# Performance work log

Hardware: AMD Instinct MI355X
Metric: run time of the kernel (lower is better)

The kernel has to match this reference:

```python
import jax, jax.numpy as jnp
from jax import lax
import numpy as np

B, T, I, H, O = 256, 1024, 64, 256, 1


def setup_inputs() -> dict:
    key = jax.random.key(0)
    ks = jax.random.split(key, 7)
    s = 0.05
    return {
        "x": jax.random.normal(ks[0], (B, T, I), dtype=jnp.float32),
        "W_ih": jax.random.normal(ks[1], (4 * H, I), dtype=jnp.float32) * s,
        "W_hh": jax.random.normal(ks[2], (4 * H, H), dtype=jnp.float32) * s,
        "b_ih": jax.random.normal(ks[3], (4 * H,), dtype=jnp.float32) * s,
        "b_hh": jax.random.normal(ks[4], (4 * H,), dtype=jnp.float32) * s,
        "fc_w": jax.random.normal(ks[5], (O, H), dtype=jnp.float32) * s,
        "fc_b": jax.random.normal(ks[6], (O,), dtype=jnp.float32) * s,
    }


def _lstm_last_hidden(x, W_ih, W_hh, b_ih, b_hh):
    # x: [B, T, I] -> last hidden state h_T: [B, H]
    h_dim = W_hh.shape[1]
    xT = jnp.swapaxes(x, 0, 1)                      # [T, B, I]
    # Precompute input contribution to gates for all timesteps (one big GEMM)
    x_gates = jnp.einsum("tbi,gi->tbg", xT, W_ih) + b_ih + b_hh  # [T, B, 4H]

    def step(carry, xg):
        h, c = carry
        g = xg + h @ W_hh.T                         # [B, 4H]
        i, f, gg, o = jnp.split(g, 4, axis=-1)       # torch gate order i,f,g,o
        i = jax.nn.sigmoid(i)
        f = jax.nn.sigmoid(f)
        gg = jnp.tanh(gg)
        o = jax.nn.sigmoid(o)
        c = f * c + i * gg
        h = o * jnp.tanh(c)
        return (h, c), None

    b = x.shape[0]
    h0 = jnp.zeros((b, h_dim), dtype=x.dtype)
    c0 = jnp.zeros((b, h_dim), dtype=x.dtype)
    (h_last, _), _ = lax.scan(step, (h0, c0), x_gates)
    return h_last


def reference(x, W_ih, W_hh, b_ih, b_hh, fc_w, fc_b):
    h_last = _lstm_last_hidden(x, W_ih, W_hh, b_ih, b_hh)  # [B, H]
    return h_last @ fc_w.T + fc_b                           # [B, O]
```

## Files before the change

### kernel.cpp

```cpp
#include <hip/hip_runtime.h>
#include <stdint.h>


#define T_ 1024
#define I_ 64
#define H_ 256
#define NSLICE 8
#define NGROUP 32
#define MB 8
#define HB 32
#define HROW 272

#define UNITS_PER_GROUP 1024
#define UNITS_PER_PARITY (NGROUP * UNITS_PER_GROUP)
#define SENT_CAP (1 << 16)

typedef float floatx4 __attribute__((ext_vector_type(4)));
typedef __bf16 bf16x8 __attribute__((ext_vector_type(8)));
typedef unsigned short ushortx8 __attribute__((ext_vector_type(8)));
typedef unsigned int uintx4 __attribute__((ext_vector_type(4)));
typedef unsigned int uint32;
typedef unsigned long long u64;

__device__ __forceinline__ float bf2f(uint32 u16) {
  uint32 u = u16 << 16;
  return __builtin_bit_cast(float, u);
}
__device__ __forceinline__ bf16x8 packbf8(floatx4 a, floatx4 b) {
  bf16x8 r;
  r[0] = (__bf16)a[0]; r[1] = (__bf16)a[1];
  r[2] = (__bf16)a[2]; r[3] = (__bf16)a[3];
  r[4] = (__bf16)b[0]; r[5] = (__bf16)b[1];
  r[6] = (__bf16)b[2]; r[7] = (__bf16)b[3];
  return r;
}
__device__ __forceinline__ float fast_sig(float v) {
  return 1.0f / (1.0f + __expf(-v));
}
__device__ __forceinline__ float fast_tanh(float v) {
  float e = __expf(2.0f * v);
  return 1.0f - 2.0f / (e + 1.0f);
}
__device__ __forceinline__ u64 aload64(const u64* p) {
  return __hip_atomic_load(p, __ATOMIC_RELAXED, __HIP_MEMORY_SCOPE_AGENT);
}
__device__ __forceinline__ void pub64(u64* p, u64 v) {
  asm volatile("global_atomic_swap_x2 %0, %1, off sc1" ::"v"(p), "v"(v)
               : "memory");
}

__global__ __launch_bounds__(256, 1) void lstm_main(
    const float* __restrict__ x, const float* __restrict__ W_ih,
    const float* __restrict__ W_hh, const float* __restrict__ b_ih,
    const float* __restrict__ b_hh, u64* __restrict__ units) {
  const int tid = threadIdx.x;
  const int bid = blockIdx.x;
  const int s = bid >> 5;
  const int g = bid & 31;
  const int w = tid >> 6;
  const int lane = tid & 63;
  const int ln = lane & 15;
  const int lk = lane >> 4;

  __shared__ float xch[4][2][16][8];
  __shared__ __align__(16) unsigned short h_lds[MB][HROW];

  {
    uint32* p = (uint32*)&h_lds[0][0];
    for (int i = tid; i < MB * HROW / 2; i += 256) p[i] = 0u;
  }

  bf16x8 wf[2][10];
  float bias[2];
#pragma unroll
  for (int j = 0; j < 2; ++j) {
    const int row = w * 256 + s * HB + j * 16 + ln;
    bias[j] = b_ih[row] + b_hh[row];
#pragma unroll
    for (int kc = 0; kc < 10; ++kc) {
      const int kk = kc * 32 + lk * 8;
      const float* src = (kk < I_) ? (W_ih + (size_t)row * I_ + kk)
                                   : (W_hh + (size_t)row * H_ + (kk - I_));
      floatx4 f0 = *(const floatx4*)src;
      floatx4 f1 = *(const floatx4*)(src + 4);
      wf[j][kc] = packbf8(f0, f1);
    }
  }

  const int mb = ln & 7;
  const float* xrow = x + ((size_t)(g * MB + mb)) * T_ * I_;
  const int um = tid >> 5;
  const int uh = tid & 31;
  const int uj = uh >> 4, un = uh & 15;
  float c_reg = 0.0f;

  const bool ownthr = (((tid & 31) >> 2) == s);

  const size_t gbase = (size_t)g * UNITS_PER_GROUP;

  __syncthreads();

#pragma unroll 1
  for (int t = 0; t < T_; ++t) {
    floatx4 xf0, xf1, xf2, xf3;
    {
      const float* src = xrow + t * I_ + lk * 8;
      xf0 = *(const floatx4*)(src);
      xf1 = *(const floatx4*)(src + 4);
      xf2 = *(const floatx4*)(src + 32);
      xf3 = *(const floatx4*)(src + 36);
    }

    const u64* up =
        units + (size_t)(t & 1) * UNITS_PER_PARITY + gbase + tid * 4;
    u64 v0 = 0, v1 = 0, v2 = 0, v3 = 0;
    const bool polling = (t > 0) && !ownthr;
    if (polling) {
      v0 = aload64(up + 0);
      v1 = aload64(up + 1);
      v2 = aload64(up + 2);
      v3 = aload64(up + 3);
    }

    bf16x8 a0 = packbf8(xf0, xf1);
    bf16x8 a1 = packbf8(xf2, xf3);
    floatx4 acc[2];
    acc[0] = (floatx4){bias[0], bias[0], bias[0], bias[0]};
    acc[1] = (floatx4){bias[1], bias[1], bias[1], bias[1]};
    acc[0] = __builtin_amdgcn_mfma_f32_16x16x32_bf16(a0, wf[0][0], acc[0],
                                                     0, 0, 0);
    acc[1] = __builtin_amdgcn_mfma_f32_16x16x32_bf16(a0, wf[1][0], acc[1],
                                                     0, 0, 0);
    acc[0] = __builtin_amdgcn_mfma_f32_16x16x32_bf16(a1, wf[0][1], acc[0],
                                                     0, 0, 0);
    acc[1] = __builtin_amdgcn_mfma_f32_16x16x32_bf16(a1, wf[1][1], acc[1],
                                                     0, 0, 0);

    if (t > 0) {
      bool ok = !polling || (((uint32)(v0 >> 32) == (uint32)t) &
                            ((uint32)(v1 >> 32) == (uint32)t) &
                            ((uint32)(v2 >> 32) == (uint32)t) &
                            ((uint32)(v3 >> 32) == (uint32)t));
      int it = 0;
      while (!__all(ok) && ++it < SENT_CAP) {
        if (!ok) {
          v0 = aload64(up + 0);
          v1 = aload64(up + 1);
          v2 = aload64(up + 2);
          v3 = aload64(up + 3);
          ok = ((uint32)(v0 >> 32) == (uint32)t) &
               ((uint32)(v1 >> 32) == (uint32)t) &
               ((uint32)(v2 >> 32) == (uint32)t) &
               ((uint32)(v3 >> 32) == (uint32)t);
        }
      }
      if (polling) {
        uintx4 d;
        d[0] = (uint32)v0; d[1] = (uint32)v1;
        d[2] = (uint32)v2; d[3] = (uint32)v3;
        uint32* dst = (uint32*)&h_lds[tid >> 5][0] + (tid & 31) * 4;
        *(uintx4*)dst = d;
      }
    }
    __syncthreads();

    const unsigned short* hrow = &h_lds[mb][0];
#pragma unroll
    for (int kc = 2; kc < 10; ++kc) {
      bf16x8 a = __builtin_bit_cast(
          bf16x8, *(const ushortx8*)(hrow + (kc - 2) * 32 + lk * 8));
      acc[0] = __builtin_amdgcn_mfma_f32_16x16x32_bf16(a, wf[0][kc], acc[0],
                                                       0, 0, 0);
      acc[1] = __builtin_amdgcn_mfma_f32_16x16x32_bf16(a, wf[1][kc], acc[1],
                                                       0, 0, 0);
    }

#pragma unroll
    for (int j = 0; j < 2; ++j) {
      floatx4 v = acc[j];
      if (w == 2) {
        v[0] = fast_tanh(v[0]); v[1] = fast_tanh(v[1]);
        v[2] = fast_tanh(v[2]); v[3] = fast_tanh(v[3]);
      } else {
        v[0] = fast_sig(v[0]); v[1] = fast_sig(v[1]);
        v[2] = fast_sig(v[2]); v[3] = fast_sig(v[3]);
      }
      if (lk < 2) {
        *(floatx4*)&xch[w][j][ln][lk * 4] = v;
      }
    }
    __syncthreads();

    float ig = xch[0][uj][un][um];
    float fg = xch[1][uj][un][um];
    float gg = xch[2][uj][un][um];
    float og = xch[3][uj][un][um];
    c_reg = fg * c_reg + ig * gg;
    float hv = og * fast_tanh(c_reg);

    unsigned short hb = __builtin_bit_cast(unsigned short, (__bf16)hv);
    int pv = __shfl_xor((int)hb, 1);
    if ((uh & 1) == 0) {
      uint32 dword = (uint32)hb | ((uint32)(unsigned short)pv << 16);
      u64 val = (u64)dword | ((u64)(uint32)(t + 1) << 32);
      u64* dst = units + (size_t)((t + 1) & 1) * UNITS_PER_PARITY + gbase +
                 (um * 128 + s * 16 + (uh >> 1));
      pub64(dst, val);
      *(uint32*)&h_lds[um][2 * (s * 16 + (uh >> 1))] = dword;
    }
  }
}

__global__ void lstm_fc(const u64* __restrict__ units,
                        const float* __restrict__ fc_w,
                        const float* __restrict__ fc_b,
                        float* __restrict__ out) {
  const int b = threadIdx.x;
  const int g = b >> 3, m = b & 7;
  const u64* base = units + (size_t)g * UNITS_PER_GROUP + m * 128;
  float sum = fc_b[0];
#pragma unroll 8
  for (int d = 0; d < 128; ++d) {
    u64 v = aload64(base + d);
    uint32 lo = (uint32)v;
    sum += bf2f(lo & 0xffffu) * fc_w[2 * d] + bf2f(lo >> 16) * fc_w[2 * d + 1];
  }
  out[b] = sum;
}

extern "C" void kernel_launch(void* const* d_in, const int* in_sizes, int n_in,
                              void* d_out, int out_size, void* d_ws,
                              size_t ws_size, hipStream_t stream) {
  const float* x    = (const float*)d_in[0];
  const float* W_ih = (const float*)d_in[1];
  const float* W_hh = (const float*)d_in[2];
  const float* b_ih = (const float*)d_in[3];
  const float* b_hh = (const float*)d_in[4];
  const float* fc_w = (const float*)d_in[5];
  const float* fc_b = (const float*)d_in[6];
  float* out = (float*)d_out;

  u64* units = (u64*)d_ws;

  lstm_main<<<dim3(NGROUP * NSLICE), dim3(256), 0, stream>>>(
      x, W_ih, W_hh, b_ih, b_hh, units);
  lstm_fc<<<dim3(1), dim3(256), 0, stream>>>(units, fc_w, fc_b, out);
}
```

Before: 2.421 ms.

## Add XCC-local fast exchange path with handshake and device-scope fallback

```diff
diff --git a/kernel.cpp b/kernel.cpp
--- a/kernel.cpp
+++ b/kernel.cpp
@@ -12,8 +12,11 @@
 #define HROW 272
 
 #define UNITS_PER_GROUP 1024
-#define UNITS_PER_PARITY (NGROUP * UNITS_PER_GROUP)
+#define UPP (NGROUP * UNITS_PER_GROUP)
 #define SENT_CAP (1 << 16)
+#define FASTCAP 24
+#define HTAG 0x48414E44u
+#define HS_CAP (1 << 20)
 
 typedef float floatx4 __attribute__((ext_vector_type(4)));
 typedef __bf16 bf16x8 __attribute__((ext_vector_type(8)));
@@ -44,9 +47,24 @@
 __device__ __forceinline__ u64 aload64(const u64* p) {
   return __hip_atomic_load(p, __ATOMIC_RELAXED, __HIP_MEMORY_SCOPE_AGENT);
 }
-__device__ __forceinline__ void pub64(u64* p, u64 v) {
-  asm volatile("global_atomic_swap_x2 %0, %1, off sc1" ::"v"(p), "v"(v)
+__device__ __forceinline__ void astore64(u64* p, u64 v) {
+  __hip_atomic_store(p, v, __ATOMIC_RELAXED, __HIP_MEMORY_SCOPE_AGENT);
+}
+__device__ __forceinline__ void pubswap(u64* p, u64 v) {
+  asm volatile("global_atomic_swap_x2 %0, %1, off" ::"v"(p), "v"(v)
                : "memory");
+}
+__device__ __forceinline__ int xcc_id() {
+  int x;
+  asm volatile("s_getreg_b32 %0, hwreg(HW_REG_XCC_ID)" : "=s"(x));
+  return x & 0xf;
+}
+__device__ __forceinline__ bool tags4(u64 v0, u64 v1, u64 v2, u64 v3,
+                                      int t) {
+  return ((uint32)(v0 >> 32) == (uint32)t) &
+         ((uint32)(v1 >> 32) == (uint32)t) &
+         ((uint32)(v2 >> 32) == (uint32)t) &
+         ((uint32)(v3 >> 32) == (uint32)t);
 }
 
 __global__ __launch_bounds__(256, 1) void lstm_main(
@@ -65,6 +83,13 @@
   __shared__ float xch[4][2][16][8];
   __shared__ __align__(16) unsigned short h_lds[MB][HROW];
 
+  const size_t gbase = (size_t)g * UNITS_PER_GROUP;
+
+  if (tid == 0) {
+    u64 hv = (u64)(uint32)xcc_id() | ((u64)HTAG << 32);
+    astore64(units + gbase + s, hv);
+  }
+
   {
     uint32* p = (uint32*)&h_lds[0][0];
     for (int i = tid; i < MB * HROW / 2; i += 256) p[i] = 0u;
@@ -87,6 +112,24 @@
     }
   }
 
+  bool fast;
+  {
+    u64 idv[8] = {0, 0, 0, 0, 0, 0, 0, 0};
+    bool hok = false;
+    for (int it = 0; !hok && it < HS_CAP; ++it) {
+      hok = true;
+#pragma unroll
+      for (int p = 0; p < 8; ++p) {
+        idv[p] = aload64(units + gbase + p);
+        hok &= ((uint32)(idv[p] >> 32) == HTAG);
+      }
+      if (!hok) __builtin_amdgcn_s_sleep(2);
+    }
+    fast = hok;
+#pragma unroll
+    for (int p = 1; p < 8; ++p) fast &= ((uint32)idv[0] == (uint32)idv[p]);
+  }
+
   const int mb = ln & 7;
   const float* xrow = x + ((size_t)(g * MB + mb)) * T_ * I_;
   const int um = tid >> 5;
@@ -95,10 +138,20 @@
   float c_reg = 0.0f;
 
   const bool ownthr = (((tid & 31) >> 2) == s);
-
-  const size_t gbase = (size_t)g * UNITS_PER_GROUP;
+  bool fastlane = fast;
 
   __syncthreads();
+
+#define FASTLOAD()                                                         \
+  asm volatile(                                                            \
+      "global_load_dwordx2 %0, %4, off sc0 nt\n\t"                         \
+      "global_load_dwordx2 %1, %4, off offset:8 sc0 nt\n\t"                \
+      "global_load_dwordx2 %2, %4, off offset:16 sc0 nt\n\t"               \
+      "global_load_dwordx2 %3, %4, off offset:24 sc0 nt\n\t"               \
+      "s_waitcnt vmcnt(0)"                                                 \
+      : "=&v"(v0), "=&v"(v1), "=&v"(v2), "=&v"(v3)                         \
+      : "v"(fup)                                                           \
+      : "memory");
 
 #pragma unroll 1
   for (int t = 0; t < T_; ++t) {
@@ -111,15 +164,16 @@
       xf3 = *(const floatx4*)(src + 36);
     }
 
-    const u64* up =
-        units + (size_t)(t & 1) * UNITS_PER_PARITY + gbase + tid * 4;
+    const u64* fup = units + (size_t)(t & 1) * UPP + gbase + tid * 4;
+    const u64* sup = fup + 2 * UPP;
     u64 v0 = 0, v1 = 0, v2 = 0, v3 = 0;
     const bool polling = (t > 0) && !ownthr;
-    if (polling) {
-      v0 = aload64(up + 0);
-      v1 = aload64(up + 1);
-      v2 = aload64(up + 2);
-      v3 = aload64(up + 3);
+    const bool pre = polling && !fastlane;
+    if (pre) {
+      v0 = aload64(sup + 0);
+      v1 = aload64(sup + 1);
+      v2 = aload64(sup + 2);
+      v3 = aload64(sup + 3);
     }
 
     bf16x8 a0 = packbf8(xf0, xf1);
@@ -137,21 +191,43 @@
                                                      0, 0, 0);
 
     if (t > 0) {
-      bool ok = !polling || (((uint32)(v0 >> 32) == (uint32)t) &
-                            ((uint32)(v1 >> 32) == (uint32)t) &
-                            ((uint32)(v2 >> 32) == (uint32)t) &
-                            ((uint32)(v3 >> 32) == (uint32)t));
-      int it = 0;
-      while (!__all(ok) && ++it < SENT_CAP) {
-        if (!ok) {
-          v0 = aload64(up + 0);
-          v1 = aload64(up + 1);
-          v2 = aload64(up + 2);
-          v3 = aload64(up + 3);
-          ok = ((uint32)(v0 >> 32) == (uint32)t) &
-               ((uint32)(v1 >> 32) == (uint32)t) &
-               ((uint32)(v2 >> 32) == (uint32)t) &
-               ((uint32)(v3 >> 32) == (uint32)t);
+      bool got = false;
+      {
+        bool fok = !(polling && fastlane);
+        if (polling && fastlane) {
+          FASTLOAD();
+          fok = tags4(v0, v1, v2, v3, t);
+        }
+        int fit = 0;
+        while (!__all(fok) && ++fit < FASTCAP) {
+          if (!fok) {
+            FASTLOAD();
+            fok = tags4(v0, v1, v2, v3, t);
+          }
+        }
+        if (polling && fastlane) {
+          if (fok) got = true;
+          else fastlane = false;
+        }
+      }
+      {
+        bool sok = !polling || got;
+        if (polling && !got && !pre) {
+          v0 = aload64(sup + 0);
+          v1 = aload64(sup + 1);
+          v2 = aload64(sup + 2);
+          v3 = aload64(sup + 3);
+        }
+        if (polling && !got) sok = tags4(v0, v1, v2, v3, t);
+        int it = 0;
+        while (!__all(sok) && ++it < SENT_CAP) {
+          if (!sok) {
+            v0 = aload64(sup + 0);
+            v1 = aload64(sup + 1);
+            v2 = aload64(sup + 2);
+            v3 = aload64(sup + 3);
+            sok = tags4(v0, v1, v2, v3, t);
+          }
         }
       }
       if (polling) {
@@ -203,12 +279,14 @@
     if ((uh & 1) == 0) {
       uint32 dword = (uint32)hb | ((uint32)(unsigned short)pv << 16);
       u64 val = (u64)dword | ((u64)(uint32)(t + 1) << 32);
-      u64* dst = units + (size_t)((t + 1) & 1) * UNITS_PER_PARITY + gbase +
-                 (um * 128 + s * 16 + (uh >> 1));
-      pub64(dst, val);
+      u64* fdst = units + (size_t)((t + 1) & 1) * UPP + gbase +
+                  (um * 128 + s * 16 + (uh >> 1));
+      if (fast) pubswap(fdst, val);
+      astore64(fdst + 2 * UPP, val);
       *(uint32*)&h_lds[um][2 * (s * 16 + (uh >> 1))] = dword;
     }
   }
+#undef FASTLOAD
 }
 
 __global__ void lstm_fc(const u64* __restrict__ units,
@@ -217,7 +295,8 @@
                         float* __restrict__ out) {
   const int b = threadIdx.x;
   const int g = b >> 3, m = b & 7;
-  const u64* base = units + (size_t)g * UNITS_PER_GROUP + m * 128;
+  const u64* base =
+      units + 2 * (size_t)UPP + (size_t)g * UNITS_PER_GROUP + m * 128;
   float sum = fc_b[0];
 #pragma unroll 8
   for (int d = 0; d < 128; ++d) {
```

Result: no change. 2.440 ms (+0.8%).
